# Performance work log

Hardware: AMD Instinct MI355X
Metric: run time of the kernel (lower is better)

## Reference

```python
import jax, jax.numpy as jnp
import numpy as np

H_DIM = 1024
GATE_DIM = 128


def setup_inputs() -> dict:
    key = jax.random.key(0)
    ks = jax.random.split(key, 7)
    B, L = 32, 2048
    bound_g = 1.0 / np.sqrt(GATE_DIM)
    bound_l = 1.0 / np.sqrt(GATE_DIM)
    return {
        "x": jax.random.normal(ks[0], (B, L, H_DIM), dtype=jnp.float32),
        # GRUCell params (PyTorch layout: rows ordered [r; z; n])
        "weight_ih": jax.random.uniform(ks[1], (3 * GATE_DIM, H_DIM), minval=-bound_g, maxval=bound_g, dtype=jnp.float32),
        "weight_hh": jax.random.uniform(ks[2], (3 * GATE_DIM, GATE_DIM), minval=-bound_g, maxval=bound_g, dtype=jnp.float32),
        "bias_ih": jax.random.uniform(ks[3], (3 * GATE_DIM,), minval=-bound_g, maxval=bound_g, dtype=jnp.float32),
        "bias_hh": jax.random.uniform(ks[4], (3 * GATE_DIM,), minval=-bound_g, maxval=bound_g, dtype=jnp.float32),
        # output linear (gate_dim -> 1)
        "lin_w": jax.random.uniform(ks[5], (1, GATE_DIM), minval=-bound_l, maxval=bound_l, dtype=jnp.float32),
        "lin_b": jax.random.uniform(ks[6], (1,), minval=-bound_l, maxval=bound_l, dtype=jnp.float32),
    }


def reference(x, weight_ih, weight_hh, bias_ih, bias_hh, lin_w, lin_b):
    """Faithful to the original PingHead.forward: `s` is never updated, so every
    timestep runs the GRUCell against a ZERO hidden state. weight_hh @ h == 0,
    leaving only bias_hh contributions. This lets us vectorize over (B, L)."""
    G = GATE_DIM
    # input projection for all gates: (B, L, 3G)
    gi = jnp.einsum('blh,gh->blg', x, weight_ih) + bias_ih
    i_r, i_z, i_n = gi[..., :G], gi[..., G:2 * G], gi[..., 2 * G:]
    b_hr, b_hz, b_hn = bias_hh[:G], bias_hh[G:2 * G], bias_hh[2 * G:]
    r = jax.nn.sigmoid(i_r + b_hr)
    z = jax.nn.sigmoid(i_z + b_hz)
    n = jnp.tanh(i_n + r * b_hn)
    h = (1.0 - z) * n  # + z * 0 (hidden state is always zero)
    # linear(gate_dim -> 1), squeeze last dim -> (B, L)
    out = jnp.einsum('blg,og->blo', h, lin_w) + lin_b
    return out[..., 0]
```

## Files before the change

### kernel.cpp

```cpp
#include <hip/hip_runtime.h>

#define H_DIM   1024
#define G_DIM   128
#define N_DIM   384
#define M_TOTAL 65536
#define BM      64
#define NSTEP   32
#define BUF_FLOATS 2048

typedef _Float16 half8  __attribute__((ext_vector_type(8)));
typedef __fp16   fp16x2 __attribute__((ext_vector_type(2)));
typedef float    f32x4  __attribute__((ext_vector_type(4)));

__device__ __forceinline__ float fast_sigmoid(float v) {
    return 1.0f / (1.0f + __expf(-v));
}
__device__ __forceinline__ float fast_tanh(float v) {
    return 1.0f - 2.0f / (__expf(2.0f * v) + 1.0f);
}

__device__ __forceinline__ half8 cvt8(f32x4 a, f32x4 b) {
    fp16x2 p0 = __builtin_amdgcn_cvt_pkrtz(a[0], a[1]);
    fp16x2 p1 = __builtin_amdgcn_cvt_pkrtz(a[2], a[3]);
    fp16x2 p2 = __builtin_amdgcn_cvt_pkrtz(b[0], b[1]);
    fp16x2 p3 = __builtin_amdgcn_cvt_pkrtz(b[2], b[3]);
    half8 h;
    h[0] = (_Float16)p0[0]; h[1] = (_Float16)p0[1];
    h[2] = (_Float16)p1[0]; h[3] = (_Float16)p1[1];
    h[4] = (_Float16)p2[0]; h[5] = (_Float16)p2[1];
    h[6] = (_Float16)p3[0]; h[7] = (_Float16)p3[1];
    return h;
}

__global__ __launch_bounds__(256) void prep_w_kernel(const float* __restrict__ w,
                                                     _Float16* __restrict__ wf) {
    int gid  = blockIdx.x * 256 + threadIdx.x;
    int lane = gid & 63;
    int fid  = gid >> 6;
    int ktg  = fid & 31;
    int ct   = fid >> 5;
    int col  = ct * 16 + (lane & 15);
    int kb   = ktg * 32 + (lane >> 4) * 8;
    const f32x4* src = (const f32x4*)(w + (size_t)col * H_DIM + kb);
    f32x4 v0 = src[0], v1 = src[1];
    half8 h;
    #pragma unroll
    for (int j = 0; j < 4; ++j) { h[j] = (_Float16)v0[j]; h[4 + j] = (_Float16)v1[j]; }
    *(half8*)(wf + (size_t)gid * 8) = h;
}

#define FENCE() asm volatile("" ::: "memory")
#define WAITV(N) { FENCE(); __builtin_amdgcn_s_waitcnt(0x0F70 | (N)); FENCE(); }
#define BARR()   { FENCE(); __builtin_amdgcn_s_barrier(); FENCE(); }

__global__ __launch_bounds__(512, 4) void ping_main_kernel(
    const float* __restrict__ x, const _Float16* __restrict__ wf,
    const float* __restrict__ bias_ih, const float* __restrict__ bias_hh,
    const float* __restrict__ lin_w, const float* __restrict__ lin_b,
    float* __restrict__ out)
{
    __shared__ float shX[4 * BUF_FLOATS];
    __shared__ float sh_out[BM];

    const int t    = threadIdx.x;
    const int lane = t & 63;
    const int wv   = t >> 6;
    const int ln   = lane & 15;
    const int quad = lane >> 4;

    if (t < BM) sh_out[t] = 0.0f;

    const size_t row0 = (size_t)blockIdx.x * BM;

    const int drow = wv * 8 + (lane >> 3);
    const int cg   = (lane & 7) ^ (2 * ((lane >> 3) & 3));
    const float* xsrc = x + (row0 + drow) * (size_t)H_DIM + cg * 4;
    float* ldsSeg = &shX[wv * 256];

#define DMA_ISSUE(K) \
    __builtin_amdgcn_global_load_lds( \
        (const __attribute__((address_space(1))) void*)(xsrc + (size_t)(K) * 32), \
        (__attribute__((address_space(3))) void*)(ldsSeg + ((K) & 3) * BUF_FLOATS), \
        16, 0, 0)

    const char* aAddr[4];
    #pragma unroll
    for (int rt = 0; rt < 4; ++rt) {
        int r  = rt * 16 + ln;
        int ce = (2 * quad) ^ (2 * (ln & 3));
        aAddr[rt] = (const char*)&shX[0] + r * 128 + ce * 16;
    }

    const _Float16* pb[3];
    #pragma unroll
    for (int i = 0; i < 3; ++i)
        pb[i] = wf + (size_t)((wv + 8 * i) * 32) * 512 + lane * 8;

    f32x4 acc[3][4];
    #pragma unroll
    for (int i = 0; i < 3; ++i)
        #pragma unroll
        for (int rt = 0; rt < 4; ++rt)
            acc[i][rt] = (f32x4){0.f, 0.f, 0.f, 0.f};

    half8 bf[2][3];

    DMA_ISSUE(0); DMA_ISSUE(1); DMA_ISSUE(2);
    #pragma unroll
    for (int i = 0; i < 3; ++i) {
        bf[0][i] = *(const half8*)(pb[i]);
        bf[1][i] = *(const half8*)(pb[i] + 512);
    }

#define ITER_BODY(KB, BUFI, WAITN, DO_ISSUE, DO_BLOAD) { \
    WAITV(WAITN); \
    BARR(); \
    if (DO_ISSUE) { DMA_ISSUE((KB) + 3); } \
    _Pragma("unroll") \
    for (int rt = 0; rt < 4; ++rt) { \
        f32x4 ve = *(const f32x4*)(aAddr[rt] + (BUFI) * 8192); \
        f32x4 vo = *(const f32x4*)(aAddr[rt] + (BUFI) * 8192 + 16); \
        half8 afr = cvt8(ve, vo); \
        _Pragma("unroll") \
        for (int i = 0; i < 3; ++i) \
            acc[i][rt] = __builtin_amdgcn_mfma_f32_16x16x32_f16(afr, bf[(BUFI) & 1][i], acc[i][rt], 0, 0, 0); \
    } \
    if (DO_BLOAD) { \
        _Pragma("unroll") \
        for (int i = 0; i < 3; ++i) \
            bf[(BUFI) & 1][i] = *(const half8*)(pb[i] + (size_t)((KB) + 2) * 512); \
    } }

    for (int kb = 0; kb < 28; kb += 4) {
        ITER_BODY(kb + 0, 0, 8, true, true);
        ITER_BODY(kb + 1, 1, 8, true, true);
        ITER_BODY(kb + 2, 2, 8, true, true);
        ITER_BODY(kb + 3, 3, 8, true, true);
    }
    ITER_BODY(28, 0, 8, true,  true);
    ITER_BODY(29, 1, 8, false, true);
    ITER_BODY(30, 2, 4, false, false);
    ITER_BODY(31, 3, 0, false, false);

    const int g = 16 * wv + ln;
    const float b_ir = bias_ih[g];
    const float b_iz = bias_ih[G_DIM + g];
    const float b_in = bias_ih[2 * G_DIM + g];
    const float b_hr = bias_hh[g];
    const float b_hz = bias_hh[G_DIM + g];
    const float b_hn = bias_hh[2 * G_DIM + g];
    const float lw   = lin_w[g];

    #pragma unroll
    for (int rt = 0; rt < 4; ++rt) {
        #pragma unroll
        for (int reg = 0; reg < 4; ++reg) {
            const float r = fast_sigmoid(acc[0][rt][reg] + b_ir + b_hr);
            const float z = fast_sigmoid(acc[1][rt][reg] + b_iz + b_hz);
            const float n = fast_tanh(acc[2][rt][reg] + b_in + r * b_hn);
            float v = lw * (1.0f - z) * n;
            v += __shfl_xor(v, 1);
            v += __shfl_xor(v, 2);
            v += __shfl_xor(v, 4);
            v += __shfl_xor(v, 8);
            if (ln == 0) atomicAdd(&sh_out[rt * 16 + quad * 4 + reg], v);
        }
    }

    __syncthreads();
    if (t < BM) out[row0 + t] = sh_out[t] + lin_b[0];
}

extern "C" void kernel_launch(void* const* d_in, const int* in_sizes, int n_in,
                              void* d_out, int out_size, void* d_ws, size_t ws_size,
                              hipStream_t stream) {
    const float* x      = (const float*)d_in[0];
    const float* w_ih   = (const float*)d_in[1];
    const float* b_ih   = (const float*)d_in[3];
    const float* b_hh   = (const float*)d_in[4];
    const float* lin_w  = (const float*)d_in[5];
    const float* lin_b  = (const float*)d_in[6];
    float* out          = (float*)d_out;
    _Float16* wf        = (_Float16*)d_ws;

    hipLaunchKernelGGL(prep_w_kernel, dim3((N_DIM / 16) * 32 * 64 / 256), dim3(256), 0, stream,
                       w_ih, wf);
    hipLaunchKernelGGL(ping_main_kernel, dim3(M_TOTAL / BM), dim3(512), 0, stream,
                       x, wf, b_ih, b_hh, lin_w, lin_b, out);
}
```

Baseline: 400.7 us.

## Stage x through registers as fp16 into double-buffered LDS instead of DMA

Result: no change. 406.5 us (+1.5%).

```diff
diff --git a/kernel.cpp b/kernel.cpp
--- a/kernel.cpp
+++ b/kernel.cpp
@@ -5,10 +5,9 @@
 #define N_DIM   384
 #define M_TOTAL 65536
 #define BM      64
-#define NSTEP   32
-#define BUF_FLOATS 2048
 
 typedef _Float16 half8  __attribute__((ext_vector_type(8)));
+typedef _Float16 half4  __attribute__((ext_vector_type(4)));
 typedef __fp16   fp16x2 __attribute__((ext_vector_type(2)));
 typedef float    f32x4  __attribute__((ext_vector_type(4)));
 
@@ -19,16 +18,12 @@
     return 1.0f - 2.0f / (__expf(2.0f * v) + 1.0f);
 }
 
-__device__ __forceinline__ half8 cvt8(f32x4 a, f32x4 b) {
-    fp16x2 p0 = __builtin_amdgcn_cvt_pkrtz(a[0], a[1]);
-    fp16x2 p1 = __builtin_amdgcn_cvt_pkrtz(a[2], a[3]);
-    fp16x2 p2 = __builtin_amdgcn_cvt_pkrtz(b[0], b[1]);
-    fp16x2 p3 = __builtin_amdgcn_cvt_pkrtz(b[2], b[3]);
-    half8 h;
+__device__ __forceinline__ half4 cvt4(f32x4 v) {
+    fp16x2 p0 = __builtin_amdgcn_cvt_pkrtz(v[0], v[1]);
+    fp16x2 p1 = __builtin_amdgcn_cvt_pkrtz(v[2], v[3]);
+    half4 h;
     h[0] = (_Float16)p0[0]; h[1] = (_Float16)p0[1];
     h[2] = (_Float16)p1[0]; h[3] = (_Float16)p1[1];
-    h[4] = (_Float16)p2[0]; h[5] = (_Float16)p2[1];
-    h[6] = (_Float16)p3[0]; h[7] = (_Float16)p3[1];
     return h;
 }
 
@@ -50,8 +45,9 @@
 }
 
 #define FENCE() asm volatile("" ::: "memory")
-#define WAITV(N) { FENCE(); __builtin_amdgcn_s_waitcnt(0x0F70 | (N)); FENCE(); }
-#define BARR()   { FENCE(); __builtin_amdgcn_s_barrier(); FENCE(); }
+#define WAITV(N)    { FENCE(); __builtin_amdgcn_s_waitcnt(0x0F70 | (N)); FENCE(); }
+#define WAITLGKM0() { FENCE(); __builtin_amdgcn_s_waitcnt(0xC07F); FENCE(); }
+#define BARRW()     { WAITLGKM0(); __builtin_amdgcn_s_barrier(); FENCE(); }
 
 __global__ __launch_bounds__(512, 4) void ping_main_kernel(
     const float* __restrict__ x, const _Float16* __restrict__ wf,
@@ -59,7 +55,7 @@
     const float* __restrict__ lin_w, const float* __restrict__ lin_b,
     float* __restrict__ out)
 {
-    __shared__ float shX[4 * BUF_FLOATS];
+    __shared__ _Float16 shX[2 * 2048];
     __shared__ float sh_out[BM];
 
     const int t    = threadIdx.x;
@@ -73,23 +69,11 @@
     const size_t row0 = (size_t)blockIdx.x * BM;
 
     const int drow = wv * 8 + (lane >> 3);
-    const int cg   = (lane & 7) ^ (2 * ((lane >> 3) & 3));
-    const float* xsrc = x + (row0 + drow) * (size_t)H_DIM + cg * 4;
-    float* ldsSeg = &shX[wv * 256];
+    const int dcol = (lane & 7) * 4;
+    const float* xsrc = x + (row0 + drow) * (size_t)H_DIM + dcol;
+    _Float16* wdst = &shX[drow * 32 + dcol];
 
-#define DMA_ISSUE(K) \
-    __builtin_amdgcn_global_load_lds( \
-        (const __attribute__((address_space(1))) void*)(xsrc + (size_t)(K) * 32), \
-        (__attribute__((address_space(3))) void*)(ldsSeg + ((K) & 3) * BUF_FLOATS), \
-        16, 0, 0)
-
-    const char* aAddr[4];
-    #pragma unroll
-    for (int rt = 0; rt < 4; ++rt) {
-        int r  = rt * 16 + ln;
-        int ce = (2 * quad) ^ (2 * (ln & 3));
-        aAddr[rt] = (const char*)&shX[0] + r * 128 + ce * 16;
-    }
+    const char* aBase = (const char*)&shX[0] + ln * 64 + quad * 16;
 
     const _Float16* pb[3];
     #pragma unroll
@@ -103,53 +87,55 @@
         for (int rt = 0; rt < 4; ++rt)
             acc[i][rt] = (f32x4){0.f, 0.f, 0.f, 0.f};
 
+    f32x4 g[2];
     half8 bf[2][3];
 
-    DMA_ISSUE(0); DMA_ISSUE(1); DMA_ISSUE(2);
+    g[0] = *(const f32x4*)(xsrc);
+    g[1] = *(const f32x4*)(xsrc + 32);
     #pragma unroll
     for (int i = 0; i < 3; ++i) {
         bf[0][i] = *(const half8*)(pb[i]);
         bf[1][i] = *(const half8*)(pb[i] + 512);
     }
+    WAITV(7);
+    *(half4*)(wdst) = cvt4(g[0]);
+    BARRW();
 
-#define ITER_BODY(KB, BUFI, WAITN, DO_ISSUE, DO_BLOAD) { \
-    WAITV(WAITN); \
-    BARR(); \
-    if (DO_ISSUE) { DMA_ISSUE((KB) + 3); } \
+#define STEP(KB, PAR, DO_PF, WAITN, DO_STAGE) { \
+    if (DO_PF) g[PAR] = *(const f32x4*)(xsrc + (size_t)((KB) + 2) * 32); \
     _Pragma("unroll") \
     for (int rt = 0; rt < 4; ++rt) { \
-        f32x4 ve = *(const f32x4*)(aAddr[rt] + (BUFI) * 8192); \
-        f32x4 vo = *(const f32x4*)(aAddr[rt] + (BUFI) * 8192 + 16); \
-        half8 afr = cvt8(ve, vo); \
+        half8 afr = *(const half8*)(aBase + (PAR) * 4096 + rt * 1024); \
         _Pragma("unroll") \
         for (int i = 0; i < 3; ++i) \
-            acc[i][rt] = __builtin_amdgcn_mfma_f32_16x16x32_f16(afr, bf[(BUFI) & 1][i], acc[i][rt], 0, 0, 0); \
+            acc[i][rt] = __builtin_amdgcn_mfma_f32_16x16x32_f16(afr, bf[PAR][i], acc[i][rt], 0, 0, 0); \
     } \
-    if (DO_BLOAD) { \
+    if (DO_PF) { \
         _Pragma("unroll") \
         for (int i = 0; i < 3; ++i) \
-            bf[(BUFI) & 1][i] = *(const half8*)(pb[i] + (size_t)((KB) + 2) * 512); \
-    } }
+            bf[PAR][i] = *(const half8*)(pb[i] + (size_t)((KB) + 2) * 512); \
+    } \
+    if (DO_STAGE) { \
+        WAITV(WAITN); \
+        *(half4*)(wdst + (((PAR) ^ 1) * 2048)) = cvt4(g[(PAR) ^ 1]); \
+    } \
+    BARRW(); }
 
-    for (int kb = 0; kb < 28; kb += 4) {
-        ITER_BODY(kb + 0, 0, 8, true, true);
-        ITER_BODY(kb + 1, 1, 8, true, true);
-        ITER_BODY(kb + 2, 2, 8, true, true);
-        ITER_BODY(kb + 3, 3, 8, true, true);
+    for (int kb = 0; kb < 30; kb += 2) {
+        STEP(kb + 0, 0, true, 7, true);
+        STEP(kb + 1, 1, true, 7, true);
     }
-    ITER_BODY(28, 0, 8, true,  true);
-    ITER_BODY(29, 1, 8, false, true);
-    ITER_BODY(30, 2, 4, false, false);
-    ITER_BODY(31, 3, 0, false, false);
+    STEP(30, 0, false, 3, true);
+    STEP(31, 1, false, 0, false);
 
-    const int g = 16 * wv + ln;
-    const float b_ir = bias_ih[g];
-    const float b_iz = bias_ih[G_DIM + g];
-    const float b_in = bias_ih[2 * G_DIM + g];
-    const float b_hr = bias_hh[g];
-    const float b_hz = bias_hh[G_DIM + g];
-    const float b_hn = bias_hh[2 * G_DIM + g];
-    const float lw   = lin_w[g];
+    const int g_col = 16 * wv + ln;
+    const float b_ir = bias_ih[g_col];
+    const float b_iz = bias_ih[G_DIM + g_col];
+    const float b_in = bias_ih[2 * G_DIM + g_col];
+    const float b_hr = bias_hh[g_col];
+    const float b_hz = bias_hh[G_DIM + g_col];
+    const float b_hn = bias_hh[2 * G_DIM + g_col];
+    const float lw   = lin_w[g_col];
 
     #pragma unroll
     for (int rt = 0; rt < 4; ++rt) {
```
